# Kernel tuning notes

Hardware: AMD Instinct MI355X
Metric: run time of the kernel (lower is better)

Reference implementation:

```python
import jax, jax.numpy as jnp
import numpy as np

N = 100000
E = 1600000
F_IN, F_HID, F_OUT = 512, 512, 256
NEG_SLOPE = 0.01  # nn.LeakyReLU default


def setup_inputs() -> dict:
    key = jax.random.key(0)
    ks = jax.random.split(key, 16)
    def lin(k, fi, fo):
        s = 1.0 / np.sqrt(fi)
        return jax.random.uniform(k, (fi, fo), jnp.float32, -s, s)
    inp = {
        'x': jax.random.normal(ks[0], (N, F_IN), jnp.float32),
        'edge_index': jax.random.randint(ks[1], (2, E), 0, N, jnp.int64),
        'W1': lin(ks[2], F_IN, F_HID), 'b1': jnp.zeros((F_HID,), jnp.float32),
        'W2': lin(ks[3], F_HID, F_HID), 'b2': jnp.zeros((F_HID,), jnp.float32),
        'W3': lin(ks[4], F_HID, F_HID), 'b3': jnp.zeros((F_HID,), jnp.float32),
        'W4': lin(ks[5], F_HID, F_OUT), 'b4': jnp.zeros((F_OUT,), jnp.float32),
        'fcW1': lin(ks[6], F_OUT, 64), 'fcb1': jnp.zeros((64,), jnp.float32),
        'fcW2': lin(ks[7], 64, 1), 'fcb2': jnp.zeros((1,), jnp.float32),
    }
    return inp


def _gcn_norm(edge_index):
    # PyG gcn_norm with add_self_loops=True: deg counts incoming edges + 1 self loop
    src, dst = edge_index[0], edge_index[1]
    deg = jax.ops.segment_sum(jnp.ones((E,), jnp.float32), dst, num_segments=N) + 1.0
    dis = jax.lax.rsqrt(deg)  # deg >= 1 always (self loops)
    edge_norm = dis[src] * dis[dst]  # [E]
    self_norm = dis * dis            # [N], norm for the added self loop
    return src, dst, edge_norm, self_norm


def _gcn_layer(x, src, dst, edge_norm, self_norm, W, b):
    xw = x @ W  # transform-then-propagate (in < out not an issue here)
    agg = jax.ops.segment_sum(xw[src] * edge_norm[:, None], dst, num_segments=N)
    return agg + self_norm[:, None] * xw + b


def leaky(x):
    return jnp.where(x >= 0, x, NEG_SLOPE * x)


def reference(x, edge_index, W1, b1, W2, b2, W3, b3, W4, b4, fcW1, fcb1, fcW2, fcb2):
    src, dst, en, sn = _gcn_norm(edge_index)
    h = leaky(_gcn_layer(x, src, dst, en, sn, W1, b1))
    h = leaky(_gcn_layer(h, src, dst, en, sn, W2, b2))
    h = leaky(_gcn_layer(h, src, dst, en, sn, W3, b3))
    h = leaky(_gcn_layer(h, src, dst, en, sn, W4, b4))
    g = jnp.mean(h, axis=0, keepdims=True)  # global_mean_pool, batch=None -> [1, F_OUT]
    g = leaky(g @ fcW1 + fcb1)
    # dropout is identity in eval mode
    g = g @ fcW2 + fcb2
    return jax.nn.sigmoid(g)  # [1, 1]
```

## Files before the change

### kernel.cpp

```cpp
#include <hip/hip_runtime.h>
#include <hip/hip_bf16.h>
#include <cstdint>
#include <cstddef>


typedef unsigned short u16;
typedef unsigned char u8;
typedef unsigned int u32;
typedef u16 u16x8 __attribute__((ext_vector_type(8)));
typedef u32 u32x2 __attribute__((ext_vector_type(2)));
typedef float f32x2 __attribute__((ext_vector_type(2)));
typedef float f32x4 __attribute__((ext_vector_type(4)));

__device__ __forceinline__ u16 f2bf(float f) {
  u32 u = __builtin_bit_cast(u32, f);
  u += 0x7fffu + ((u >> 16) & 1u);
  return (u16)(u >> 16);
}
__device__ __forceinline__ float bf2f(u16 h) {
  return __builtin_bit_cast(float, (u32)h << 16);
}
__device__ __forceinline__ void g2lds16(const void* g, void* l) {
  __builtin_amdgcn_global_load_lds((__attribute__((address_space(1))) void*)g,
                                   (__attribute__((address_space(3))) void*)l, 16, 0, 0);
}

__global__ __launch_bounds__(256) void init_kernel(int* __restrict__ deg,
                                                   int* __restrict__ cursor,
                                                   float* __restrict__ pool, int N) {
  int i = blockIdx.x * 256 + threadIdx.x;
  if (i < N) { deg[i] = 0; cursor[i] = 0; }
  if (i < 256) pool[i] = 0.f;
}

__global__ void detect_kernel(const int* __restrict__ ei, int* __restrict__ flag) {
  __shared__ int nz;
  if (threadIdx.x == 0) nz = 0;
  __syncthreads();
  if (ei[2 * threadIdx.x + 1] != 0) atomicAdd(&nz, 1);
  __syncthreads();
  if (threadIdx.x == 0) *flag = (nz == 0) ? 1 : 0;
}

__device__ __forceinline__ int ld_src(const int* ei, int E, int e, int f64) {
  return f64 ? (int)((const long long*)ei)[e] : ei[e];
}
__device__ __forceinline__ int ld_dst(const int* ei, int E, int e, int f64) {
  return f64 ? (int)((const long long*)ei)[(long long)E + e] : ei[E + e];
}

__global__ __launch_bounds__(256) void degree_kernel(const int* __restrict__ ei,
                                                     const int* __restrict__ flag,
                                                     int* __restrict__ deg, int E) {
  int e = blockIdx.x * 256 + threadIdx.x;
  if (e >= E) return;
  int f = *flag;
  atomicAdd(&deg[ld_dst(ei, E, e, f)], 1);
}

__global__ __launch_bounds__(256) void dis_kernel(const int* __restrict__ deg,
                                                  float* __restrict__ dis, int N) {
  int i = blockIdx.x * 256 + threadIdx.x;
  if (i < N) dis[i] = rsqrtf((float)deg[i] + 1.0f);
}

__global__ __launch_bounds__(1024) void scan1_kernel(const int* __restrict__ deg,
                                                     int* __restrict__ rs,
                                                     int* __restrict__ bsum, int N) {
  __shared__ int s[1024];
  int tid = threadIdx.x;
  int i = blockIdx.x * 1024 + tid;
  int v = (i < N) ? deg[i] : 0;
  s[tid] = v;
  __syncthreads();
  for (int off = 1; off < 1024; off <<= 1) {
    int t = (tid >= off) ? s[tid - off] : 0;
    __syncthreads();
    s[tid] += t;
    __syncthreads();
  }
  if (i < N) rs[i] = s[tid] - v;
  if (tid == 1023) bsum[blockIdx.x] = s[1023];
}

__global__ __launch_bounds__(1024) void scan2_kernel(const int* __restrict__ bsum,
                                                     int* __restrict__ boff, int nb) {
  __shared__ int s[1024];
  int tid = threadIdx.x;
  int v = (tid < nb) ? bsum[tid] : 0;
  s[tid] = v;
  __syncthreads();
  for (int off = 1; off < 1024; off <<= 1) {
    int t = (tid >= off) ? s[tid - off] : 0;
    __syncthreads();
    s[tid] += t;
    __syncthreads();
  }
  if (tid < nb) boff[tid] = s[tid] - v;
}

__global__ __launch_bounds__(256) void scan3_kernel(int* __restrict__ rs,
                                                    const int* __restrict__ boff, int N) {
  int i = blockIdx.x * 256 + threadIdx.x;
  if (i < N) rs[i] += boff[i >> 10];
}

__global__ __launch_bounds__(256) void fill_kernel(const int* __restrict__ ei,
                                                   const int* __restrict__ flag,
                                                   const int* __restrict__ rs,
                                                   int* __restrict__ cursor,
                                                   int* __restrict__ colv, int E) {
  int e = blockIdx.x * 256 + threadIdx.x;
  if (e >= E) return;
  int f = *flag;
  int s = ld_src(ei, E, e, f);
  int d = ld_dst(ei, E, e, f);
  int p = atomicAdd(&cursor[d], 1);
  colv[rs[d] + p] = s;
}

__global__ __launch_bounds__(256) void convx_kernel(const float* __restrict__ x,
                                                    u8* __restrict__ x8, size_t n) {
  size_t i = ((size_t)blockIdx.x * 256 + threadIdx.x) * 4;
  if (i >= n) return;
  float4 v = *reinterpret_cast<const float4*>(x + i);
  int lo = __builtin_amdgcn_cvt_pk_fp8_f32(v.x, v.y, 0, false);
  int r = __builtin_amdgcn_cvt_pk_fp8_f32(v.z, v.w, lo, true);
  *reinterpret_cast<u32*>(x8 + i) = (u32)r;
}

__global__ __launch_bounds__(256) void convw_kernel(const float* __restrict__ W,
                                                    u8* __restrict__ Wt, int Nout) {
  int id = blockIdx.x * 256 + threadIdx.x;
  if (id >= 512 * Nout) return;
  int k = id / Nout, n = id - k * Nout;
  float v = W[id];
  int e = __builtin_amdgcn_cvt_pk_fp8_f32(v, v, 0, false);
  Wt[n * 512 + k] = (u8)e;
}

template <bool OUT8, bool BACT>
__global__ __launch_bounds__(256, 2)
void gemm8_kernel(const u8* __restrict__ A, const u8* __restrict__ Bt,
                  void* __restrict__ Cout, const float* __restrict__ bias,
                  int M, int Nout) {
  __shared__ u8 sA[128 * 32];
  __shared__ u8 sB[128 * 32];
  const int tid = threadIdx.x;
  const int wave = tid >> 6, lane = tid & 63;
  const int m0 = blockIdx.x * 128;
  const int n0 = blockIdx.y * 128;
  const int wm = (wave >> 1) * 64, wn = (wave & 1) * 64;
  const int srow = wave * 32 + (lane >> 1);
  const int soff = (lane & 1) * 16;
  const int fr = lane & 15, fq8 = (lane >> 4) * 8;

  f32x4 acc[4][4];
#pragma unroll
  for (int i = 0; i < 4; ++i)
#pragma unroll
    for (int j = 0; j < 4; ++j) acc[i][j] = (f32x4){0.f, 0.f, 0.f, 0.f};

  for (int k0 = 0; k0 < 512; k0 += 32) {
    {
      int arow = m0 + srow;
      arow = arow < M ? arow : M - 1;
      g2lds16(A + (size_t)arow * 512 + k0 + soff, &sA[(wave * 32) * 32]);
      int brow = n0 + srow;
      g2lds16(Bt + (size_t)brow * 512 + k0 + soff, &sB[(wave * 32) * 32]);
    }
    __builtin_amdgcn_s_waitcnt(0);
    __syncthreads();

    long long af[4], bf[4];
#pragma unroll
    for (int t = 0; t < 4; ++t) {
      af[t] = *reinterpret_cast<const long long*>(&sA[(wm + t * 16 + fr) * 32 + fq8]);
      bf[t] = *reinterpret_cast<const long long*>(&sB[(wn + t * 16 + fr) * 32 + fq8]);
    }
#pragma unroll
    for (int i = 0; i < 4; ++i)
#pragma unroll
      for (int j = 0; j < 4; ++j)
        acc[i][j] = __builtin_amdgcn_mfma_f32_16x16x32_fp8_fp8(af[i], bf[j], acc[i][j], 0, 0, 0);
    __syncthreads();
  }

  const int crow0 = m0 + wm + ((lane >> 4) << 2);
  const int ccol0 = n0 + wn + (lane & 15);
#pragma unroll
  for (int j = 0; j < 4; ++j) {
    const int col = ccol0 + j * 16;
    float bj = BACT ? bias[col] : 0.f;
#pragma unroll
    for (int i = 0; i < 4; ++i)
#pragma unroll
      for (int r = 0; r < 4; ++r) {
        int row = crow0 + i * 16 + r;
        if (row < M) {
          float v = acc[i][j][r];
          if (BACT) { v += bj; v = v >= 0.f ? v : 0.01f * v; }
          if (OUT8) {
            int e = __builtin_amdgcn_cvt_pk_fp8_f32(v, v, 0, false);
            ((u8*)Cout)[(size_t)row * Nout + col] = (u8)e;
          } else {
            ((u16*)Cout)[(size_t)row * Nout + col] = f2bf(v);
          }
        }
      }
  }
}

template <bool ACT>
__global__ __launch_bounds__(256)
void agg_kernel(const u8* __restrict__ xw, const int* __restrict__ colv,
                const int* __restrict__ rs, const int* __restrict__ deg,
                const float* __restrict__ dis, const float* __restrict__ bias,
                u8* __restrict__ hout, int N) {
  const int wave = threadIdx.x >> 6;
  const int lane = threadIdx.x & 63;
  const int node = blockIdx.x * 4 + wave;
  if (node >= N) return;
  const int start = rs[node];
  const int d = deg[node];
  const float dd = dis[node];
  const int fo = lane * 8;

  f32x2 acc[4];
#pragma unroll
  for (int i = 0; i < 4; ++i) acc[i] = (f32x2){0.f, 0.f};

  const int total = d + 1;
  for (int base = 0; base < total; base += 64) {
    int t = base + lane;
    int s = node;
    float w = 0.f;
    if (t < d)       { s = colv[start + t]; w = dd * dis[s]; }
    else if (t == d) { w = dd * dd; }
    int cnt = total - base;
    if (cnt > 64) cnt = 64;
    int cnt8 = (cnt + 7) & ~7;
    int wi = __builtin_bit_cast(int, w);
    for (int j = 0; j < cnt8; j += 8) {
      u32x2 v[8];
      float ws[8];
#pragma unroll
      for (int k = 0; k < 8; ++k) {
        int sk = __builtin_amdgcn_readlane(s, j + k);
        ws[k] = __builtin_bit_cast(float, __builtin_amdgcn_readlane(wi, j + k));
        v[k] = *reinterpret_cast<const u32x2*>(xw + (size_t)sk * 512 + fo);
      }
#pragma unroll
      for (int k = 0; k < 8; ++k) {
        f32x2 p0 = __builtin_amdgcn_cvt_pk_f32_fp8((int)v[k].x, false);
        f32x2 p1 = __builtin_amdgcn_cvt_pk_f32_fp8((int)v[k].x, true);
        f32x2 p2 = __builtin_amdgcn_cvt_pk_f32_fp8((int)v[k].y, false);
        f32x2 p3 = __builtin_amdgcn_cvt_pk_f32_fp8((int)v[k].y, true);
        f32x2 wv = (f32x2){ws[k], ws[k]};
        acc[0] += wv * p0;
        acc[1] += wv * p1;
        acc[2] += wv * p2;
        acc[3] += wv * p3;
      }
    }
  }

  float h[8];
#pragma unroll
  for (int i = 0; i < 8; ++i) {
    float v = (i & 1) ? acc[i >> 1].y : acc[i >> 1].x;
    if (ACT) { v += bias[fo + i]; v = v >= 0.f ? v : 0.01f * v; }
    h[i] = v;
  }
  int lo = __builtin_amdgcn_cvt_pk_fp8_f32(h[0], h[1], 0, false);
  lo = __builtin_amdgcn_cvt_pk_fp8_f32(h[2], h[3], lo, true);
  int hi = __builtin_amdgcn_cvt_pk_fp8_f32(h[4], h[5], 0, false);
  hi = __builtin_amdgcn_cvt_pk_fp8_f32(h[6], h[7], hi, true);
  u32x2 o; o.x = (u32)lo; o.y = (u32)hi;
  __builtin_nontemporal_store(o, reinterpret_cast<u32x2*>(hout + (size_t)node * 512 + fo));
}

__global__ __launch_bounds__(256) void pool_kernel(const u16* __restrict__ h,
                                                   float* __restrict__ pool, int N) {
  __shared__ float lds[8 * 256];
  const int tid = threadIdx.x;
  const int fg = tid & 31;
  const int rg = tid >> 5;
  float acc[8];
#pragma unroll
  for (int i = 0; i < 8; ++i) acc[i] = 0.f;
  for (int r = blockIdx.x * 8 + rg; r < N; r += gridDim.x * 8) {
    u16x8 v = *reinterpret_cast<const u16x8*>(h + (size_t)r * 256 + fg * 8);
#pragma unroll
    for (int i = 0; i < 8; ++i) acc[i] += bf2f(v[i]);
  }
#pragma unroll
  for (int i = 0; i < 8; ++i) lds[rg * 256 + fg * 8 + i] = acc[i];
  __syncthreads();
  float s = 0.f;
#pragma unroll
  for (int g = 0; g < 8; ++g) s += lds[g * 256 + tid];
  atomicAdd(&pool[tid], s);
}

__global__ void fc_kernel(const float* __restrict__ pool, const float* __restrict__ fcW1,
                          const float* __restrict__ fcb1, const float* __restrict__ fcW2,
                          const float* __restrict__ fcb2, float* __restrict__ out,
                          float invN) {
  int j = threadIdx.x;
  float acc = 0.f;
  for (int f = 0; f < 256; ++f) acc += pool[f] * invN * fcW1[f * 64 + j];
  float h = acc + fcb1[j];
  h = h >= 0.f ? h : 0.01f * h;
  float p = h * fcW2[j];
  for (int o = 32; o; o >>= 1) p += __shfl_down(p, o);
  if (j == 0) out[0] = 1.f / (1.f + expf(-(p + fcb2[0])));
}

extern "C" void kernel_launch(void* const* d_in, const int* in_sizes, int n_in,
                              void* d_out, int out_size, void* d_ws, size_t ws_size,
                              hipStream_t stream) {
  const float* x    = (const float*)d_in[0];
  const int*   ei   = (const int*)d_in[1];
  const float* W1   = (const float*)d_in[2];
  const float* b1   = (const float*)d_in[3];
  const float* W2   = (const float*)d_in[4];
  const float* b2   = (const float*)d_in[5];
  const float* W3   = (const float*)d_in[6];
  const float* b3   = (const float*)d_in[7];
  const float* W4   = (const float*)d_in[8];
  const float* b4   = (const float*)d_in[9];
  const float* fcW1 = (const float*)d_in[10];
  const float* fcb1 = (const float*)d_in[11];
  const float* fcW2 = (const float*)d_in[12];
  const float* fcb2 = (const float*)d_in[13];
  float* out = (float*)d_out;

  const int N = in_sizes[0] / 512;
  const int E = in_sizes[1] / 2;

  char* p = (char*)d_ws;
  auto carve = [&](size_t bytes) {
    char* r = p;
    p += (bytes + 255) & ~(size_t)255;
    return r;
  };
  u8*  bufX = (u8*)carve((size_t)N * 512);
  u8*  bufP = (u8*)carve((size_t)N * 512);
  u8*  bufQ = (u8*)carve((size_t)N * 512);
  u16* bufH4 = (u16*)carve((size_t)N * 256 * 2);
  u8* Wt1 = (u8*)carve(512 * 512);
  u8* Wt2 = (u8*)carve(512 * 512);
  u8* Wt3 = (u8*)carve(512 * 512);
  u8* Wt4 = (u8*)carve(512 * 256);
  int* deg    = (int*)carve((size_t)N * 4);
  int* cursor = (int*)carve((size_t)N * 4);
  int* rs     = (int*)carve((size_t)(N + 1) * 4);
  int* colv   = (int*)carve((size_t)E * 4);
  int* bsum   = (int*)carve(1024 * 4);
  int* boff   = (int*)carve(1024 * 4);
  int* flag   = (int*)carve(256);
  float* disv = (float*)carve((size_t)N * 4);
  float* pool = (float*)carve(256 * 4);
  if ((size_t)(p - (char*)d_ws) > ws_size) return;

  const int nb1024 = (N + 1023) / 1024;

  init_kernel<<<(N + 255) / 256, 256, 0, stream>>>(deg, cursor, pool, N);
  detect_kernel<<<1, 256, 0, stream>>>(ei, flag);
  degree_kernel<<<(E + 255) / 256, 256, 0, stream>>>(ei, flag, deg, E);
  dis_kernel<<<(N + 255) / 256, 256, 0, stream>>>(deg, disv, N);
  scan1_kernel<<<nb1024, 1024, 0, stream>>>(deg, rs, bsum, N);
  scan2_kernel<<<1, 1024, 0, stream>>>(bsum, boff, nb1024);
  scan3_kernel<<<(N + 255) / 256, 256, 0, stream>>>(rs, boff, N);
  fill_kernel<<<(E + 255) / 256, 256, 0, stream>>>(ei, flag, rs, cursor, colv, E);

  convx_kernel<<<((size_t)N * 512 / 4 + 255) / 256, 256, 0, stream>>>(x, bufX, (size_t)N * 512);
  convw_kernel<<<(512 * 512 + 255) / 256, 256, 0, stream>>>(W1, Wt1, 512);
  convw_kernel<<<(512 * 512 + 255) / 256, 256, 0, stream>>>(W2, Wt2, 512);
  convw_kernel<<<(512 * 512 + 255) / 256, 256, 0, stream>>>(W3, Wt3, 512);
  convw_kernel<<<(512 * 256 + 255) / 256, 256, 0, stream>>>(W4, Wt4, 256);

  const unsigned gm = (unsigned)((N + 127) / 128);
  const unsigned ga = (unsigned)((N + 3) / 4);

  gemm8_kernel<true, false><<<dim3(gm, 4), 256, 0, stream>>>(bufX, Wt1, bufP, nullptr, N, 512);
  agg_kernel<true><<<ga, 256, 0, stream>>>(bufP, colv, rs, deg, disv, b1, bufQ, N);
  gemm8_kernel<true, false><<<dim3(gm, 4), 256, 0, stream>>>(bufQ, Wt2, bufP, nullptr, N, 512);
  agg_kernel<true><<<ga, 256, 0, stream>>>(bufP, colv, rs, deg, disv, b2, bufX, N);
  gemm8_kernel<true, false><<<dim3(gm, 4), 256, 0, stream>>>(bufX, Wt3, bufP, nullptr, N, 512);
  agg_kernel<true><<<ga, 256, 0, stream>>>(bufP, colv, rs, deg, disv, b3, bufQ, N);
  agg_kernel<false><<<ga, 256, 0, stream>>>(bufQ, colv, rs, deg, disv, nullptr, bufX, N);
  gemm8_kernel<false, true><<<dim3(gm, 2), 256, 0, stream>>>(bufX, Wt4, bufH4, b4, N, 256);

  pool_kernel<<<256, 256, 0, stream>>>(bufH4, pool, N);
  fc_kernel<<<1, 64, 0, stream>>>(pool, fcW1, fcb1, fcW2, fcb2, out, 1.0f / (float)N);
}
```

Before: 1.278 ms.

## Swizzle fp8 layouts, widen GEMM K-tile, transform-then-aggregate for layer four

All fp8 activation and weight buffers now use an XOR swizzle, (row&7)<<3 applied to the column. It is applied when writing from convx, convw, the GEMM epilogue and the aggregation stores, and undone on the gather loads. The aim is to remove LDS bank conflicts when the GEMM reads MFMA fragments. The GEMM K-tile grows from 32 to 64, so each barrier now covers twice as many MFMAs. The last layer switches from aggregate-then-transform to transform-then-aggregate, so its gather runs over 256-wide rows instead of 512-wide ones. Bias and LeakyReLU for that layer move into a new agg256 kernel. The cost is more index arithmetic on every access and double the shared-memory tile size.

```diff
diff --git a/kernel.cpp b/kernel.cpp
--- a/kernel.cpp
+++ b/kernel.cpp
@@ -7,6 +7,7 @@
 typedef unsigned short u16;
 typedef unsigned char u8;
 typedef unsigned int u32;
+typedef u16 u16x4 __attribute__((ext_vector_type(4)));
 typedef u16 u16x8 __attribute__((ext_vector_type(8)));
 typedef u32 u32x2 __attribute__((ext_vector_type(2)));
 typedef float f32x2 __attribute__((ext_vector_type(2)));
@@ -126,34 +127,36 @@
   float4 v = *reinterpret_cast<const float4*>(x + i);
   int lo = __builtin_amdgcn_cvt_pk_fp8_f32(v.x, v.y, 0, false);
   int r = __builtin_amdgcn_cvt_pk_fp8_f32(v.z, v.w, lo, true);
-  *reinterpret_cast<u32*>(x8 + i) = (u32)r;
+  size_t row = i >> 9;
+  int col = (int)(i & 511);
+  int sw = ((int)(row & 7)) << 3;
+  *reinterpret_cast<u32*>(x8 + row * 512 + (col ^ sw)) = (u32)r;
 }
 
 __global__ __launch_bounds__(256) void convw_kernel(const float* __restrict__ W,
                                                     u8* __restrict__ Wt, int Nout) {
   int id = blockIdx.x * 256 + threadIdx.x;
   if (id >= 512 * Nout) return;
-  int k = id / Nout, n = id - k * Nout;
+  int k = id / Nout, nn = id - k * Nout;
   float v = W[id];
   int e = __builtin_amdgcn_cvt_pk_fp8_f32(v, v, 0, false);
-  Wt[n * 512 + k] = (u8)e;
-}
-
-template <bool OUT8, bool BACT>
+  Wt[nn * 512 + (k ^ ((nn & 7) << 3))] = (u8)e;
+}
+
 __global__ __launch_bounds__(256, 2)
 void gemm8_kernel(const u8* __restrict__ A, const u8* __restrict__ Bt,
-                  void* __restrict__ Cout, const float* __restrict__ bias,
-                  int M, int Nout) {
-  __shared__ u8 sA[128 * 32];
-  __shared__ u8 sB[128 * 32];
+                  u8* __restrict__ Cout, int M, int Nout) {
+  __shared__ u8 sA[128 * 64];
+  __shared__ u8 sB[128 * 64];
   const int tid = threadIdx.x;
   const int wave = tid >> 6, lane = tid & 63;
   const int m0 = blockIdx.x * 128;
   const int n0 = blockIdx.y * 128;
   const int wm = (wave >> 1) * 64, wn = (wave & 1) * 64;
-  const int srow = wave * 32 + (lane >> 1);
-  const int soff = (lane & 1) * 16;
+  const int srow = tid >> 2;
+  const int soff = (tid & 3) * 16;
   const int fr = lane & 15, fq8 = (lane >> 4) * 8;
+  const int xa = (fr & 7) << 3;
 
   f32x4 acc[4][4];
 #pragma unroll
@@ -161,28 +164,39 @@
 #pragma unroll
     for (int j = 0; j < 4; ++j) acc[i][j] = (f32x4){0.f, 0.f, 0.f, 0.f};
 
-  for (int k0 = 0; k0 < 512; k0 += 32) {
-    {
-      int arow = m0 + srow;
-      arow = arow < M ? arow : M - 1;
-      g2lds16(A + (size_t)arow * 512 + k0 + soff, &sA[(wave * 32) * 32]);
-      int brow = n0 + srow;
-      g2lds16(Bt + (size_t)brow * 512 + k0 + soff, &sB[(wave * 32) * 32]);
+  int ar0 = m0 + srow;      if (ar0 >= M) ar0 = M - 1;
+  int ar1 = m0 + 64 + srow; if (ar1 >= M) ar1 = M - 1;
+  const size_t a0 = (size_t)ar0 * 512 + soff;
+  const size_t a1 = (size_t)ar1 * 512 + soff;
+  const size_t b0 = (size_t)(n0 + srow) * 512 + soff;
+  const size_t b1 = (size_t)(n0 + 64 + srow) * 512 + soff;
+
+  for (int k0 = 0; k0 < 512; k0 += 64) {
+    g2lds16(A + a0 + k0, &sA[wave * 1024]);
+    g2lds16(A + a1 + k0, &sA[4096 + wave * 1024]);
+    g2lds16(Bt + b0 + k0, &sB[wave * 1024]);
+    g2lds16(Bt + b1 + k0, &sB[4096 + wave * 1024]);
+    __builtin_amdgcn_s_waitcnt(0);
+    __syncthreads();
+
+    long long af[2][4], bf[2][4];
+#pragma unroll
+    for (int t = 0; t < 4; ++t) {
+      const int ra = (wm + t * 16 + fr) * 64;
+      const int rb = (wn + t * 16 + fr) * 64;
+#pragma unroll
+      for (int s = 0; s < 2; ++s) {
+        af[s][t] = *reinterpret_cast<const long long*>(&sA[ra + ((s * 32 + fq8) ^ xa)]);
+        bf[s][t] = *reinterpret_cast<const long long*>(&sB[rb + ((s * 32 + fq8) ^ xa)]);
+      }
     }
-    __builtin_amdgcn_s_waitcnt(0);
-    __syncthreads();
-
-    long long af[4], bf[4];
-#pragma unroll
-    for (int t = 0; t < 4; ++t) {
-      af[t] = *reinterpret_cast<const long long*>(&sA[(wm + t * 16 + fr) * 32 + fq8]);
-      bf[t] = *reinterpret_cast<const long long*>(&sB[(wn + t * 16 + fr) * 32 + fq8]);
-    }
 #pragma unroll
     for (int i = 0; i < 4; ++i)
 #pragma unroll
-      for (int j = 0; j < 4; ++j)
-        acc[i][j] = __builtin_amdgcn_mfma_f32_16x16x32_fp8_fp8(af[i], bf[j], acc[i][j], 0, 0, 0);
+      for (int j = 0; j < 4; ++j) {
+        acc[i][j] = __builtin_amdgcn_mfma_f32_16x16x32_fp8_fp8(af[0][i], bf[0][j], acc[i][j], 0, 0, 0);
+        acc[i][j] = __builtin_amdgcn_mfma_f32_16x16x32_fp8_fp8(af[1][i], bf[1][j], acc[i][j], 0, 0, 0);
+      }
     __syncthreads();
   }
 
@@ -191,7 +205,6 @@
 #pragma unroll
   for (int j = 0; j < 4; ++j) {
     const int col = ccol0 + j * 16;
-    float bj = BACT ? bias[col] : 0.f;
 #pragma unroll
     for (int i = 0; i < 4; ++i)
 #pragma unroll
@@ -199,19 +212,13 @@
         int row = crow0 + i * 16 + r;
         if (row < M) {
           float v = acc[i][j][r];
-          if (BACT) { v += bj; v = v >= 0.f ? v : 0.01f * v; }
-          if (OUT8) {
-            int e = __builtin_amdgcn_cvt_pk_fp8_f32(v, v, 0, false);
-            ((u8*)Cout)[(size_t)row * Nout + col] = (u8)e;
-          } else {
-            ((u16*)Cout)[(size_t)row * Nout + col] = f2bf(v);
-          }
+          int e = __builtin_amdgcn_cvt_pk_fp8_f32(v, v, 0, false);
+          Cout[(size_t)row * Nout + (col ^ ((row & 7) << 3))] = (u8)e;
         }
       }
   }
 }
 
-template <bool ACT>
 __global__ __launch_bounds__(256)
 void agg_kernel(const u8* __restrict__ xw, const int* __restrict__ colv,
                 const int* __restrict__ rs, const int* __restrict__ deg,
@@ -248,7 +255,7 @@
       for (int k = 0; k < 8; ++k) {
         int sk = __builtin_amdgcn_readlane(s, j + k);
         ws[k] = __builtin_bit_cast(float, __builtin_amdgcn_readlane(wi, j + k));
-        v[k] = *reinterpret_cast<const u32x2*>(xw + (size_t)sk * 512 + fo);
+        v[k] = *reinterpret_cast<const u32x2*>(xw + (size_t)sk * 512 + (fo ^ ((sk & 7) << 3)));
       }
 #pragma unroll
       for (int k = 0; k < 8; ++k) {
@@ -269,7 +276,8 @@
 #pragma unroll
   for (int i = 0; i < 8; ++i) {
     float v = (i & 1) ? acc[i >> 1].y : acc[i >> 1].x;
-    if (ACT) { v += bias[fo + i]; v = v >= 0.f ? v : 0.01f * v; }
+    v += bias[fo + i];
+    v = v >= 0.f ? v : 0.01f * v;
     h[i] = v;
   }
   int lo = __builtin_amdgcn_cvt_pk_fp8_f32(h[0], h[1], 0, false);
@@ -277,7 +285,68 @@
   int hi = __builtin_amdgcn_cvt_pk_fp8_f32(h[4], h[5], 0, false);
   hi = __builtin_amdgcn_cvt_pk_fp8_f32(h[6], h[7], hi, true);
   u32x2 o; o.x = (u32)lo; o.y = (u32)hi;
-  __builtin_nontemporal_store(o, reinterpret_cast<u32x2*>(hout + (size_t)node * 512 + fo));
+  __builtin_nontemporal_store(o, reinterpret_cast<u32x2*>(
+      hout + (size_t)node * 512 + (fo ^ ((node & 7) << 3))));
+}
+
+__global__ __launch_bounds__(256)
+void agg256_kernel(const u8* __restrict__ xw, const int* __restrict__ colv,
+                   const int* __restrict__ rs, const int* __restrict__ deg,
+                   const float* __restrict__ dis, const float* __restrict__ bias,
+                   u16* __restrict__ hout, int N) {
+  const int wave = threadIdx.x >> 6;
+  const int lane = threadIdx.x & 63;
+  const int node = blockIdx.x * 4 + wave;
+  if (node >= N) return;
+  const int start = rs[node];
+  const int d = deg[node];
+  const float dd = dis[node];
+  const int fo = lane * 4;
+
+  f32x2 acc[2];
+  acc[0] = (f32x2){0.f, 0.f};
+  acc[1] = (f32x2){0.f, 0.f};
+
+  const int total = d + 1;
+  for (int base = 0; base < total; base += 64) {
+    int t = base + lane;
+    int s = node;
+    float w = 0.f;
+    if (t < d)       { s = colv[start + t]; w = dd * dis[s]; }
+    else if (t == d) { w = dd * dd; }
+    int cnt = total - base;
+    if (cnt > 64) cnt = 64;
+    int cnt8 = (cnt + 7) & ~7;
+    int wi = __builtin_bit_cast(int, w);
+    for (int j = 0; j < cnt8; j += 8) {
+      u32 v[8];
+      float ws[8];
+#pragma unroll
+      for (int k = 0; k < 8; ++k) {
+        int sk = __builtin_amdgcn_readlane(s, j + k);
+        ws[k] = __builtin_bit_cast(float, __builtin_amdgcn_readlane(wi, j + k));
+        v[k] = *reinterpret_cast<const u32*>(xw + (size_t)sk * 256 + (fo ^ ((sk & 7) << 3)));
+      }
+#pragma unroll
+      for (int k = 0; k < 8; ++k) {
+        f32x2 p0 = __builtin_amdgcn_cvt_pk_f32_fp8((int)v[k], false);
+        f32x2 p1 = __builtin_amdgcn_cvt_pk_f32_fp8((int)v[k], true);
+        f32x2 wv = (f32x2){ws[k], ws[k]};
+        acc[0] += wv * p0;
+        acc[1] += wv * p1;
+      }
+    }
+  }
+
+  u16x4 o;
+#pragma unroll
+  for (int i = 0; i < 4; ++i) {
+    float v = (i & 1) ? acc[i >> 1].y : acc[i >> 1].x;
+    v += bias[fo + i];
+    v = v >= 0.f ? v : 0.01f * v;
+    o[i] = f2bf(v);
+  }
+  *reinterpret_cast<u16x4*>(hout + (size_t)node * 256 + fo) = o;
 }
 
 __global__ __launch_bounds__(256) void pool_kernel(const u16* __restrict__ h,
@@ -384,14 +453,14 @@
   const unsigned gm = (unsigned)((N + 127) / 128);
   const unsigned ga = (unsigned)((N + 3) / 4);
 
-  gemm8_kernel<true, false><<<dim3(gm, 4), 256, 0, stream>>>(bufX, Wt1, bufP, nullptr, N, 512);
-  agg_kernel<true><<<ga, 256, 0, stream>>>(bufP, colv, rs, deg, disv, b1, bufQ, N);
-  gemm8_kernel<true, false><<<dim3(gm, 4), 256, 0, stream>>>(bufQ, Wt2, bufP, nullptr, N, 512);
-  agg_kernel<true><<<ga, 256, 0, stream>>>(bufP, colv, rs, deg, disv, b2, bufX, N);
-  gemm8_kernel<true, false><<<dim3(gm, 4), 256, 0, stream>>>(bufX, Wt3, bufP, nullptr, N, 512);
-  agg_kernel<true><<<ga, 256, 0, stream>>>(bufP, colv, rs, deg, disv, b3, bufQ, N);
-  agg_kernel<false><<<ga, 256, 0, stream>>>(bufQ, colv, rs, deg, disv, nullptr, bufX, N);
-  gemm8_kernel<false, true><<<dim3(gm, 2), 256, 0, stream>>>(bufX, Wt4, bufH4, b4, N, 256);
+  gemm8_kernel<<<dim3(gm, 4), 256, 0, stream>>>(bufX, Wt1, bufP, N, 512);
+  agg_kernel<<<ga, 256, 0, stream>>>(bufP, colv, rs, deg, disv, b1, bufQ, N);
+  gemm8_kernel<<<dim3(gm, 4), 256, 0, stream>>>(bufQ, Wt2, bufP, N, 512);
+  agg_kernel<<<ga, 256, 0, stream>>>(bufP, colv, rs, deg, disv, b2, bufX, N);
+  gemm8_kernel<<<dim3(gm, 4), 256, 0, stream>>>(bufX, Wt3, bufP, N, 512);
+  agg_kernel<<<ga, 256, 0, stream>>>(bufP, colv, rs, deg, disv, b3, bufQ, N);
+  gemm8_kernel<<<dim3(gm, 2), 256, 0, stream>>>(bufQ, Wt4, bufP, N, 256);
+  agg256_kernel<<<ga, 256, 0, stream>>>(bufP, colv, rs, deg, disv, b4, bufH4, N);
 
   pool_kernel<<<256, 256, 0, stream>>>(bufH4, pool, N);
   fc_kernel<<<1, 64, 0, stream>>>(pool, fcW1, fcb1, fcW2, fcb2, out, 1.0f / (float)N);
```

Result: faster. 1.137 ms (-11.0%).
